# Optimization experiments

Hardware: AMD Instinct MI355X
Metric: run time of the kernel (lower is better)

## Reference

```python
import jax, jax.numpy as jnp
import numpy as np

B, D_IN, H, T = 8192, 5000, 512, 16

def setup_inputs() -> dict:
    key = jax.random.key(0)
    ks = jax.random.split(key, 7)
    s_mlp = 1.0 / np.sqrt(D_IN)
    s_cla = 1.0 / np.sqrt(H)
    return {
        "data_input": jax.random.normal(ks[0], (B, D_IN), jnp.float32),
        "mlp_w": jax.random.normal(ks[1], (H, D_IN), jnp.float32) * s_mlp,
        "mlp_b": jax.random.normal(ks[2], (H,), jnp.float32) * s_mlp,
        "CM": jax.random.normal(ks[3], (T, H, H), jnp.float32) * (1.0 / np.sqrt(H)),
        "attn": jax.random.normal(ks[4], (H, T), jnp.float32) * (1.0 / np.sqrt(H)),
        "cla_w": jax.random.normal(ks[5], (1, H), jnp.float32) * s_cla,
        "cla_b": jax.random.normal(ks[6], (1,), jnp.float32) * s_cla,
    }

def reference(data_input, mlp_w, mlp_b, CM, attn, cla_w, cla_b):
    # mlp_out: [B,H]  (dropout p=0 -> identity)
    mlp_out = data_input @ mlp_w.T + mlp_b
    # task attention weights: softmax over tasks, [B,T]
    w = jax.nn.softmax(mlp_out @ attn, axis=1)
    # Fused mixture-of-matrices apply: out[b,k] = sum_t w[b,t] * sum_h mlp_out[b,h] * CM[t,h,k]
    # Avoids materializing the [B,T,H,H] tensor of the original.
    btk = jnp.einsum('bh,thk->btk', mlp_out, CM)   # [B,T,H]
    mlp_out_1 = jnp.einsum('bt,btk->bk', w, btk)   # [B,H]
    # classifier + sigmoid, squeeze -> [B]
    logits = mlp_out_1 @ cla_w.T + cla_b           # [B,1]
    return jax.nn.sigmoid(logits)[:, 0]
```

## Files before the change

kernel.cpp:

```cpp
#include <hip/hip_runtime.h>
#include <hip/hip_bf16.h>
#include <stdint.h>

typedef __bf16 bf16x8 __attribute__((ext_vector_type(8)));
typedef float f32x4 __attribute__((ext_vector_type(4)));


__device__ __forceinline__ void gld_lds16(const void* g, void* l) {
  __builtin_amdgcn_global_load_lds(
      (const __attribute__((address_space(1))) unsigned int*)g,
      (__attribute__((address_space(3))) unsigned int*)l, 16, 0, 0);
}

__device__ __forceinline__ uint16_t f2bf(float f) {
  uint32_t u = __float_as_uint(f);
  return (uint16_t)((u + 0x7fffu + ((u >> 16) & 1u)) >> 16);
}

__device__ __forceinline__ uint32_t pk2(float a, float b) {
  return (uint32_t)f2bf(a) | ((uint32_t)f2bf(b) << 16);
}

__global__ void cast_pad_kernel(const float* __restrict__ in,
                                uint16_t* __restrict__ out,
                                int rows, int cin, int cout) {
  int64_t idx = (int64_t)blockIdx.x * 256 + threadIdx.x;
  int perRow = cout >> 3;
  int64_t total = (int64_t)rows * perRow;
  if (idx >= total) return;
  int r = (int)(idx / perRow);
  int k = ((int)(idx % perRow)) << 3;
  uint4 v;
  if (k < cin) {
    const float4* p = (const float4*)(in + (int64_t)r * cin + k);
    float4 f0 = p[0], f1 = p[1];
    v = make_uint4(pk2(f0.x, f0.y), pk2(f0.z, f0.w),
                   pk2(f1.x, f1.y), pk2(f1.z, f1.w));
  } else {
    v = make_uint4(0u, 0u, 0u, 0u);
  }
  *(uint4*)(out + (int64_t)r * cout + k) = v;
}

__global__ void init_bias(const float* __restrict__ bias,
                          float* __restrict__ MO) {
  int i = blockIdx.x * 256 + threadIdx.x;
  float4 bv = ((const float4*)bias)[i & 127];
  ((float4*)MO)[i] = bv;
}

__global__ __launch_bounds__(256, 2) void gemm1_split(
    const uint16_t* __restrict__ A, const uint16_t* __restrict__ Bm,
    float* __restrict__ C, int M, int N, int K, int kChunk) {
  __shared__ __align__(16) uint16_t As[128 * 64];
  __shared__ __align__(16) uint16_t Bs[128 * 64];
  const int tid = threadIdx.x;
  const int lane = tid & 63;
  const int wid = tid >> 6;
  const int wm = wid >> 1, wn = wid & 1;

  const int lin = blockIdx.x;
  const int mlo = lin & 7;
  const int nbk = (lin >> 3) & 3;
  const int rest = lin >> 5;
  const int m0 = ((rest & 7) * 8 + mlo) * 128;
  const int n0 = nbk * 128;
  const int k0 = (rest >> 3) * kChunk;

  const int srow = tid >> 3;
  const int skswz = ((tid & 7) ^ (srow & 7)) << 3;
  const uint16_t* Ab = A + (int64_t)(m0 + srow) * K + skswz;
  const uint16_t* Bb = Bm + (int64_t)(n0 + srow) * K + skswz;

  const int lrow = lane & 15;
  const int key = lrow & 7;
  const int kg = lane >> 4;

  f32x4 acc[4][4] = {};

  for (int kt = k0; kt < k0 + kChunk; kt += 64) {
#pragma unroll
    for (int p = 0; p < 4; ++p)
      gld_lds16(Ab + (int64_t)(p * 32) * K + kt, &As[(p * 256 + tid) * 8]);
#pragma unroll
    for (int p = 0; p < 4; ++p)
      gld_lds16(Bb + (int64_t)(p * 32) * K + kt, &Bs[(p * 256 + tid) * 8]);
    __syncthreads();
#pragma unroll
    for (int ks = 0; ks < 2; ++ks) {
      const int off = (((ks << 2) | kg) ^ key) << 3;
      bf16x8 af[4], bfr[4];
#pragma unroll
      for (int i = 0; i < 4; ++i)
        af[i] = *(const bf16x8*)&As[(wm * 64 + i * 16 + lrow) * 64 + off];
#pragma unroll
      for (int j = 0; j < 4; ++j)
        bfr[j] = *(const bf16x8*)&Bs[(wn * 64 + j * 16 + lrow) * 64 + off];
#pragma unroll
      for (int i = 0; i < 4; ++i)
#pragma unroll
        for (int j = 0; j < 4; ++j)
          acc[i][j] = __builtin_amdgcn_mfma_f32_16x16x32_bf16(af[i], bfr[j],
                                                              acc[i][j], 0, 0, 0);
    }
    __syncthreads();
  }

  const int r0 = (lane >> 4) << 2;
#pragma unroll
  for (int i = 0; i < 4; ++i) {
    int row = m0 + wm * 64 + i * 16 + r0;
#pragma unroll
    for (int j = 0; j < 4; ++j) {
      int col = n0 + wn * 64 + j * 16 + (lane & 15);
      float* cp = C + (int64_t)row * N + col;
#pragma unroll
      for (int r = 0; r < 4; ++r) unsafeAtomicAdd(&cp[(int64_t)r * N], acc[i][j][r]);
    }
  }
}

__global__ __launch_bounds__(256) void cmv_kernel(const float* __restrict__ CM,
                                                  const float* __restrict__ cla_w,
                                                  float* __restrict__ Vs) {
  const int tid = threadIdx.x, lane = tid & 63, wid = tid >> 6;
  const int row = blockIdx.x * 4 + wid;
  const float4* src = (const float4*)(CM + (int64_t)row * 512);
  const float4* cw = (const float4*)cla_w;
  float4 a0 = src[lane * 2], a1 = src[lane * 2 + 1];
  float4 w0 = cw[lane * 2], w1 = cw[lane * 2 + 1];
  float s = a0.x * w0.x + a0.y * w0.y + a0.z * w0.z + a0.w * w0.w +
            a1.x * w1.x + a1.y * w1.y + a1.z * w1.z + a1.w * w1.w;
#pragma unroll
  for (int o = 32; o >= 1; o >>= 1) s += __shfl_xor(s, o);
  if (lane == 0) {
    int t = row >> 9, h = row & 511;
    Vs[h * 16 + t] = s;
  }
}

__global__ __launch_bounds__(256) void attn_final(
    const float* __restrict__ MO, const float* __restrict__ attn,
    const float* __restrict__ Vs, const float* __restrict__ cla_b,
    float* __restrict__ out) {
  __shared__ float xs[16 * 512];
  __shared__ float avs[256 * 32];
  const int tid = threadIdx.x;
  const int b0 = blockIdx.x * 16;
#pragma unroll
  for (int p = 0; p < 8; ++p) {
    int e4 = p * 256 + tid;
    ((float4*)xs)[e4] = ((const float4*)(MO + (int64_t)b0 * 512))[e4];
  }
  const int lane = tid & 63, w = tid >> 6;
  const int bl = w * 4 + (lane >> 4);
  const int t = lane & 15;
  const float* xr = xs + bl * 512;
  float s = 0.f, y = 0.f;
  for (int ph = 0; ph < 2; ++ph) {
    __syncthreads();
#pragma unroll
    for (int p = 0; p < 4; ++p) {
      int e4 = p * 256 + tid;
      int h = e4 >> 2, c = (e4 & 3) << 2;
      *(float4*)&avs[h * 32 + c] = ((const float4*)attn)[ph * 1024 + e4];
      *(float4*)&avs[h * 32 + 16 + c] = ((const float4*)Vs)[ph * 1024 + e4];
    }
    __syncthreads();
    const float* xp = xr + ph * 256;
#pragma unroll 4
    for (int h = 0; h < 256; ++h) {
      float xv = xp[h];
      s += xv * avs[h * 32 + t];
      y += xv * avs[h * 32 + 16 + t];
    }
  }
  float m = s;
#pragma unroll
  for (int o = 8; o >= 1; o >>= 1) m = fmaxf(m, __shfl_xor(m, o));
  float e = __expf(s - m);
  float sum = e;
#pragma unroll
  for (int o = 8; o >= 1; o >>= 1) sum += __shfl_xor(sum, o);
  float val = (e / sum) * y;
#pragma unroll
  for (int o = 8; o >= 1; o >>= 1) val += __shfl_xor(val, o);
  if (t == 0) out[b0 + bl] = 1.f / (1.f + __expf(-(val + cla_b[0])));
}

extern "C" void kernel_launch(void* const* d_in, const int* in_sizes, int n_in,
                              void* d_out, int out_size, void* d_ws,
                              size_t ws_size, hipStream_t stream) {
  const float* data = (const float*)d_in[0];
  const float* mlp_w = (const float*)d_in[1];
  const float* mlp_b = (const float*)d_in[2];
  const float* CM = (const float*)d_in[3];
  const float* attn = (const float*)d_in[4];
  const float* cla_w = (const float*)d_in[5];
  const float* cla_b = (const float*)d_in[6];
  float* out = (float*)d_out;

  char* ws = (char*)d_ws;
  uint16_t* Xb = (uint16_t*)(ws + 0);
  uint16_t* Wb = (uint16_t*)(ws + 83886080);
  float* MO = (float*)(ws + 89128960);
  float* Vs = (float*)(ws + 0);

  cast_pad_kernel<<<20480, 256, 0, stream>>>(data, Xb, 8192, 5000, 5120);
  cast_pad_kernel<<<1280, 256, 0, stream>>>(mlp_w, Wb, 512, 5000, 5120);
  init_bias<<<4096, 256, 0, stream>>>(mlp_b, MO);
  gemm1_split<<<1280, 256, 0, stream>>>(Xb, Wb, MO, 8192, 512, 5120, 1024);
  cmv_kernel<<<2048, 256, 0, stream>>>(CM, cla_w, Vs);
  attn_final<<<512, 256, 0, stream>>>(MO, attn, Vs, cla_b, out);
}
```

Baseline: 377.9 us.

## Fuse fp32-to-bf16 activation cast into GEMM and replace atomics with split-K partials

Drops the separate cast/pad pass over the large activation matrix. The GEMM now reads fp32 rows directly, converts them to bf16 in registers and writes them into swizzled LDS, avoiding a full round-trip of an intermediate bf16 copy. Split-K goes from 5 atomic chunks to 3 partial buffers written with plain stores, and the bias add and partial reduction move into the final attention kernel, which removes init_bias. The cost is that A is no longer loaded asynchronously straight into LDS, so load latency is exposed through registers, and the occupancy hint rises to 3.

```diff
diff --git a/kernel.cpp b/kernel.cpp
--- a/kernel.cpp
+++ b/kernel.cpp
@@ -19,6 +19,13 @@
 
 __device__ __forceinline__ uint32_t pk2(float a, float b) {
   return (uint32_t)f2bf(a) | ((uint32_t)f2bf(b) << 16);
+}
+
+__device__ __forceinline__ uint32_t pkbf(float a, float b) {
+  __hip_bfloat162 h = __float22bfloat162_rn(make_float2(a, b));
+  union { __hip_bfloat162 h2; uint32_t u; } cv;
+  cv.h2 = h;
+  return cv.u;
 }
 
 __global__ void cast_pad_kernel(const float* __restrict__ in,
@@ -42,16 +49,10 @@
   *(uint4*)(out + (int64_t)r * cout + k) = v;
 }
 
-__global__ void init_bias(const float* __restrict__ bias,
-                          float* __restrict__ MO) {
-  int i = blockIdx.x * 256 + threadIdx.x;
-  float4 bv = ((const float4*)bias)[i & 127];
-  ((float4*)MO)[i] = bv;
-}
-
-__global__ __launch_bounds__(256, 2) void gemm1_split(
-    const uint16_t* __restrict__ A, const uint16_t* __restrict__ Bm,
-    float* __restrict__ C, int M, int N, int K, int kChunk) {
+__global__ __launch_bounds__(256, 3) void gemm1_fused(
+    const float* __restrict__ A,
+    const uint16_t* __restrict__ Bm,
+    float* __restrict__ P) {
   __shared__ __align__(16) uint16_t As[128 * 64];
   __shared__ __align__(16) uint16_t Bs[128 * 64];
   const int tid = threadIdx.x;
@@ -63,14 +64,21 @@
   const int mlo = lin & 7;
   const int nbk = (lin >> 3) & 3;
   const int rest = lin >> 5;
-  const int m0 = ((rest & 7) * 8 + mlo) * 128;
+  const int mhi = rest & 7;
+  const int z = rest >> 3;
+  const int m0 = (mhi * 8 + mlo) * 128;
   const int n0 = nbk * 128;
-  const int k0 = (rest >> 3) * kChunk;
+  const int it0 = (z == 0) ? 0 : (27 + 26 * (z - 1));
+  const int itN = (z == 0) ? 27 : 26;
+
+  const int arow = tid >> 1;
+  const int ahalf = tid & 1;
+  const int akey = arow & 7;
+  const float* Arow = A + (int64_t)(m0 + arow) * 5000;
 
   const int srow = tid >> 3;
   const int skswz = ((tid & 7) ^ (srow & 7)) << 3;
-  const uint16_t* Ab = A + (int64_t)(m0 + srow) * K + skswz;
-  const uint16_t* Bb = Bm + (int64_t)(n0 + srow) * K + skswz;
+  const uint16_t* Bb = Bm + (int64_t)(n0 + srow) * 5056 + skswz;
 
   const int lrow = lane & 15;
   const int key = lrow & 7;
@@ -78,13 +86,22 @@
 
   f32x4 acc[4][4] = {};
 
-  for (int kt = k0; kt < k0 + kChunk; kt += 64) {
+  for (int it = 0; it < itN; ++it) {
+    const int kt = (it0 + it) << 6;
 #pragma unroll
     for (int p = 0; p < 4; ++p)
-      gld_lds16(Ab + (int64_t)(p * 32) * K + kt, &As[(p * 256 + tid) * 8]);
-#pragma unroll
-    for (int p = 0; p < 4; ++p)
-      gld_lds16(Bb + (int64_t)(p * 32) * K + kt, &Bs[(p * 256 + tid) * 8]);
+      gld_lds16(Bb + (int64_t)(p * 32) * 5056 + kt, &Bs[(p * 256 + tid) * 8]);
+#pragma unroll
+    for (int q = 0; q < 4; ++q) {
+      const int c = ahalf * 4 + q;
+      const int g = c ^ akey;
+      const int col = kt + (g << 3);
+      const float4* s = (const float4*)(Arow + (col < 5000 ? col : 0));
+      float4 f0 = s[0], f1 = s[1];
+      uint4 v = make_uint4(pkbf(f0.x, f0.y), pkbf(f0.z, f0.w),
+                           pkbf(f1.x, f1.y), pkbf(f1.z, f1.w));
+      *(uint4*)&As[arow * 64 + c * 8] = v;
+    }
     __syncthreads();
 #pragma unroll
     for (int ks = 0; ks < 2; ++ks) {
@@ -106,6 +123,7 @@
     __syncthreads();
   }
 
+  float* Pz = P + (int64_t)z * 8192 * 512;
   const int r0 = (lane >> 4) << 2;
 #pragma unroll
   for (int i = 0; i < 4; ++i) {
@@ -113,9 +131,9 @@
 #pragma unroll
     for (int j = 0; j < 4; ++j) {
       int col = n0 + wn * 64 + j * 16 + (lane & 15);
-      float* cp = C + (int64_t)row * N + col;
-#pragma unroll
-      for (int r = 0; r < 4; ++r) unsafeAtomicAdd(&cp[(int64_t)r * N], acc[i][j][r]);
+      float* cp = Pz + (int64_t)row * 512 + col;
+#pragma unroll
+      for (int r = 0; r < 4; ++r) cp[(int64_t)r * 512] = acc[i][j][r];
     }
   }
 }
@@ -140,17 +158,30 @@
 }
 
 __global__ __launch_bounds__(256) void attn_final(
-    const float* __restrict__ MO, const float* __restrict__ attn,
-    const float* __restrict__ Vs, const float* __restrict__ cla_b,
-    float* __restrict__ out) {
+    const float* __restrict__ P,
+    const float* __restrict__ bias,
+    const float* __restrict__ attn, const float* __restrict__ Vs,
+    const float* __restrict__ cla_b, float* __restrict__ out) {
   __shared__ float xs[16 * 512];
   __shared__ float avs[256 * 32];
   const int tid = threadIdx.x;
   const int b0 = blockIdx.x * 16;
+  const int64_t base4 = (int64_t)b0 * 128;
+  const float4* P0 = (const float4*)P;
+  const float4* P1 = P0 + (int64_t)8192 * 128;
+  const float4* P2 = P1 + (int64_t)8192 * 128;
+  const float4* b4 = (const float4*)bias;
 #pragma unroll
   for (int p = 0; p < 8; ++p) {
     int e4 = p * 256 + tid;
-    ((float4*)xs)[e4] = ((const float4*)(MO + (int64_t)b0 * 512))[e4];
+    float4 a = P0[base4 + e4], b = P1[base4 + e4], c = P2[base4 + e4];
+    float4 bb = b4[e4 & 127];
+    float4 r;
+    r.x = a.x + b.x + c.x + bb.x;
+    r.y = a.y + b.y + c.y + bb.y;
+    r.z = a.z + b.z + c.z + bb.z;
+    r.w = a.w + b.w + c.w + bb.w;
+    ((float4*)xs)[e4] = r;
   }
   const int lane = tid & 63, w = tid >> 6;
   const int bl = w * 4 + (lane >> 4);
@@ -201,15 +232,12 @@
   float* out = (float*)d_out;
 
   char* ws = (char*)d_ws;
-  uint16_t* Xb = (uint16_t*)(ws + 0);
-  uint16_t* Wb = (uint16_t*)(ws + 83886080);
-  float* MO = (float*)(ws + 89128960);
-  float* Vs = (float*)(ws + 0);
-
-  cast_pad_kernel<<<20480, 256, 0, stream>>>(data, Xb, 8192, 5000, 5120);
-  cast_pad_kernel<<<1280, 256, 0, stream>>>(mlp_w, Wb, 512, 5000, 5120);
-  init_bias<<<4096, 256, 0, stream>>>(mlp_b, MO);
-  gemm1_split<<<1280, 256, 0, stream>>>(Xb, Wb, MO, 8192, 512, 5120, 1024);
+  uint16_t* Wb = (uint16_t*)(ws + 0);
+  float* P = (float*)(ws + 5177344);
+  float* Vs = (float*)(ws + 55508992);
+
+  cast_pad_kernel<<<1264, 256, 0, stream>>>(mlp_w, Wb, 512, 5000, 5056);
   cmv_kernel<<<2048, 256, 0, stream>>>(CM, cla_w, Vs);
-  attn_final<<<512, 256, 0, stream>>>(MO, attn, Vs, cla_b, out);
-}
+  gemm1_fused<<<768, 256, 0, stream>>>(data, Wb, P);
+  attn_final<<<512, 256, 0, stream>>>(P, mlp_b, attn, Vs, cla_b, out);
+}
```

After: 411.4 us. +8.9%, slower.
